# Performance work log

Measured on AMD Instinct MI355X. Metric: run time of the kernel, lower is better.

## Reference

```python
import jax, jax.numpy as jnp
import numpy as np

N, R, D = 2048, 4, 256
TEMPERATURE = 1.0
CLAMP_MIN = 1e-8


def setup_inputs() -> dict:
    key = jax.random.key(0)
    a = jax.random.normal(key, (N, R, D), dtype=jnp.float32)
    return {"a": a}


def reference(a):
    n, r, d = a.shape
    # Full pairwise Gram tensor over (input i, context j) x (input k, context l)
    sim = jnp.einsum('ijd,kld->ikjl', a, a) / TEMPERATURE          # [N,N,r,r]
    # detached row-max over l for stability (matches sim.detach().max(-1, keepdim=True))
    sim_max = jax.lax.stop_gradient(jnp.max(sim, axis=-1, keepdims=True))
    dp = jnp.exp(sim - sim_max)                                    # [N,N,r,r]

    # Positive pairs: i == k, j != l
    diag = jnp.einsum('iijl->ijl', dp)                             # [N,r,r]
    offdiag_jl = ~jnp.eye(r, dtype=bool)                           # [r,r]
    sim_pos = jnp.sum(diag * offdiag_jl, axis=(1, 2)) / (r * (r - 1))  # [N]

    # Negative pairs: i != k, all (j,l); square then clamp, then per-i mean
    sq = jnp.maximum(jnp.square(dp), CLAMP_MIN)                    # [N,N,r,r]
    diag_sq = jnp.sum(jnp.maximum(jnp.square(diag), CLAMP_MIN), axis=(1, 2))  # [N]
    sim_neg = (jnp.sum(sq, axis=(1, 2, 3)) - diag_sq) / ((n - 1) * r * r)     # [N]

    lora_loss = -2.0 * sim_pos + sim_neg                           # [N]
    return jnp.mean(lora_loss)                                     # 'mean' reduction -> scalar
```

## Files before the change

### kernel.cpp

```cpp
#include <hip/hip_runtime.h>


#define PD   8192
#define KB   256
#define BM   128
#define BK   32
#define NIT  (KB / BK)

typedef __bf16 bf16x8 __attribute__((ext_vector_type(8)));
typedef float f32x4 __attribute__((ext_vector_type(4)));

__device__ __forceinline__ void gload16(const void* g, void* l) {
    __builtin_amdgcn_global_load_lds(
        (const __attribute__((address_space(1))) unsigned int*)g,
        (__attribute__((address_space(3))) unsigned int*)l, 16, 0, 0);
}

__device__ __forceinline__ int swz(int row) { return ((row >> 1) & 3) << 4; }

__device__ __forceinline__ float quadmax(float x) {
    int v = __builtin_amdgcn_mov_dpp(__builtin_bit_cast(int, x), 0xB1, 0xF, 0xF, true);
    float m = fmaxf(x, __builtin_bit_cast(float, v));
    v = __builtin_amdgcn_mov_dpp(__builtin_bit_cast(int, m), 0x4E, 0xF, 0xF, true);
    return fmaxf(m, __builtin_bit_cast(float, v));
}

__global__ __launch_bounds__(256)
void cvt_bf16(const float* __restrict__ A, __bf16* __restrict__ W,
              float* __restrict__ out) {
    const int idx = blockIdx.x * 256 + threadIdx.x;
    if (idx == 0) *out = 0.f;
    const float4 v0 = reinterpret_cast<const float4*>(A)[idx * 2];
    const float4 v1 = reinterpret_cast<const float4*>(A)[idx * 2 + 1];
    bf16x8 h;
    h[0] = (__bf16)v0.x; h[1] = (__bf16)v0.y; h[2] = (__bf16)v0.z; h[3] = (__bf16)v0.w;
    h[4] = (__bf16)v1.x; h[5] = (__bf16)v1.y; h[6] = (__bf16)v1.z; h[7] = (__bf16)v1.w;
    *reinterpret_cast<bf16x8*>(W + (size_t)idx * 8) = h;
}

__global__ __launch_bounds__(256)
void evd_mfma(const __bf16* __restrict__ W, float* __restrict__ out)
{
    __shared__ __bf16 lds[2][2][BM * BK];
    __shared__ float wsum[4];

    const int x = blockIdx.x, y = blockIdx.y;
    int bi, bk;
    if (x < 64 - y) { bi = y;      bk = y + x; }
    else            { bi = 63 - y; bk = x - 1; }

    const int tid = threadIdx.x;
    const int lane = tid & 63, wid = tid >> 6;
    const int wr = wid >> 1, wc = wid & 1;
    const int row0 = bi * BM, col0 = bk * BM;

    const int r0 = tid >> 2;
    const int r1 = 64 + r0;
    const int x0 = (tid & 3) * 16;
    const int ga0 = r0 * (KB * 2) + (x0 ^ swz(r0));
    const int ga1 = r1 * (KB * 2) + (x0 ^ swz(r1));
    const char* gAb = (const char*)(W + (size_t)row0 * KB);
    const char* gBb = (const char*)(W + (size_t)col0 * KB);
    const int ldsOff0 = wid * 1024;
    const int ldsOff1 = 4096 + wid * 1024;

    const int fr = lane & 15, kq = lane >> 4;
    int aOff[4], bOff[4];
#pragma unroll
    for (int m = 0; m < 4; ++m) {
        const int ra = wr * 64 + m * 16 + fr;
        const int rb = wc * 64 + m * 16 + fr;
        aOff[m] = ra * 64 + ((kq * 16) ^ swz(ra));
        bOff[m] = rb * 64 + ((kq * 16) ^ swz(rb));
    }

    f32x4 acc[4][4];
#pragma unroll
    for (int m = 0; m < 4; ++m)
#pragma unroll
        for (int n = 0; n < 4; ++n)
#pragma unroll
            for (int q = 0; q < 4; ++q) acc[m][n][q] = 0.f;

    auto stage = [&](int t, int b) {
        const int kbyte = t * (BK * 2);
        char* dA = (char*)&lds[b][0][0];
        char* dB = (char*)&lds[b][1][0];
        gload16(gAb + ga0 + kbyte, dA + ldsOff0);
        gload16(gAb + ga1 + kbyte, dA + ldsOff1);
        gload16(gBb + ga0 + kbyte, dB + ldsOff0);
        gload16(gBb + ga1 + kbyte, dB + ldsOff1);
    };

    stage(0, 0);
    stage(1, 1);

#pragma unroll
    for (int t = 0; t < NIT; ++t) {
        if (t == NIT - 1) asm volatile("s_waitcnt vmcnt(0)" ::: "memory");
        else              asm volatile("s_waitcnt vmcnt(4)" ::: "memory");
        __builtin_amdgcn_s_barrier();

        const char* baseA = (const char*)&lds[t & 1][0][0];
        const char* baseB = (const char*)&lds[t & 1][1][0];
        bf16x8 af[4], bfr[4];
#pragma unroll
        for (int m = 0; m < 4; ++m) {
            af[m]  = *(const bf16x8*)(baseA + aOff[m]);
            bfr[m] = *(const bf16x8*)(baseB + bOff[m]);
        }
        if (t + 2 < NIT) {
            asm volatile("s_waitcnt lgkmcnt(0)" ::: "memory");
            __builtin_amdgcn_s_barrier();
            stage(t + 2, t & 1);
        }
#pragma unroll
        for (int m = 0; m < 4; ++m)
#pragma unroll
            for (int n = 0; n < 4; ++n)
                acc[m][n] = __builtin_amdgcn_mfma_f32_16x16x32_bf16(af[m], bfr[n], acc[m][n], 0, 0, 0);
    }

    const float C_NEG = 1.0f / (2048.0f * 2047.0f * 16.0f);
    const float C_POS = 2.0f / (2048.0f * 12.0f);
    const float SCL = 2.0f * 1.4426950408889634f;
    const bool diag = (bi == bk);
    const bool ik = ((lane >> 4) == ((lane & 15) >> 2));
    float nsum = 0.f, psum = 0.f;

#pragma unroll
    for (int m = 0; m < 4; ++m) {
#pragma unroll
        for (int n = 0; n < 4; ++n) {
            float yv[4];
#pragma unroll
            for (int q = 0; q < 4; ++q) yv[q] = SCL * acc[m][n][q];
            const bool dfrag = diag && (wr == wc) && (m == n);
#pragma unroll
            for (int r = 0; r < 4; ++r) {
                const float d2 = yv[r] - quadmax(yv[r]);
                if (dfrag) {
                    const float dp = __builtin_amdgcn_exp2f(0.5f * d2);
                    if (ik) {
                        if (r != (lane & 3)) psum += dp;
                    } else {
                        nsum += fmaxf(dp * dp, 1e-8f);
                    }
                } else {
                    nsum += fmaxf(__builtin_amdgcn_exp2f(d2), 1e-8f);
                }
            }
            if (!diag) {
                const float ymax = fmaxf(fmaxf(fmaxf(yv[0], yv[1]), yv[2]), yv[3]);
#pragma unroll
                for (int r = 0; r < 4; ++r)
                    nsum += fmaxf(__builtin_amdgcn_exp2f(yv[r] - ymax), 1e-8f);
            }
        }
    }

    float contrib = C_NEG * nsum - C_POS * psum;

#pragma unroll
    for (int off = 32; off; off >>= 1) contrib += __shfl_down(contrib, off);
    if ((tid & 63) == 0) wsum[tid >> 6] = contrib;
    __syncthreads();
    if (tid == 0) atomicAdd(out, wsum[0] + wsum[1] + wsum[2] + wsum[3]);
}

extern "C" void kernel_launch(void* const* d_in, const int* in_sizes, int n_in,
                              void* d_out, int out_size, void* d_ws, size_t ws_size,
                              hipStream_t stream) {
    const float* A = (const float*)d_in[0];
    float* out = (float*)d_out;
    __bf16* W = (__bf16*)d_ws;
    cvt_bf16<<<(PD * KB / 8) / 256, 256, 0, stream>>>(A, W, out);
    dim3 grid(65, 32);
    evd_mfma<<<grid, 256, 0, stream>>>(W, out);
}
```

Measured before the change: 98.96 us.

## Pair adjacent column tiles per block sharing one A tile across eight waves

Each block now has 512 threads and computes two neighbouring 128x128 upper-triangle tiles that share the same row tile. The A tile is loaded into LDS once and serves both halves, which cuts global-to-LDS traffic per tile. A new block-id remap spreads work across XCDs, and s_setprio raises wave priority around the MFMA loop. The cost is more LDS per block (three tile slices per buffer), and some blocks carry an invalid right tile whose work is computed and then discarded.

New measurement: 92.82 us. 6.2% less time.

```diff
diff --git a/kernel.cpp b/kernel.cpp
--- a/kernel.cpp
+++ b/kernel.cpp
@@ -38,31 +38,48 @@
     *reinterpret_cast<bf16x8*>(W + (size_t)idx * 8) = h;
 }
 
-__global__ __launch_bounds__(256)
+__global__ __launch_bounds__(512)
 void evd_mfma(const __bf16* __restrict__ W, float* __restrict__ out)
 {
-    __shared__ __bf16 lds[2][2][BM * BK];
-    __shared__ float wsum[4];
-
-    const int x = blockIdx.x, y = blockIdx.y;
-    int bi, bk;
-    if (x < 64 - y) { bi = y;      bk = y + x; }
-    else            { bi = 63 - y; bk = x - 1; }
+    __shared__ __bf16 lds[2][3][BM * BK];
+    __shared__ float wsum[8];
+
+    const int nid = (blockIdx.z * gridDim.y + blockIdx.y) * gridDim.x + blockIdx.x;
+    const int id  = (nid & 7) * 132 + (nid >> 3);
+    const int xx  = id % 33;
+    const int yzq = id / 33;
+    const int yy  = yzq & 15;
+    const int zz  = yzq >> 4;
+    int rp, px;
+    if (xx < 32 - yy) { rp = yy;      px = xx; }
+    else              { rp = 31 - yy; px = xx - (32 - yy); }
+    const int bi  = 2 * rp + zz;
+    const int bkL = bi + 2 * px;
+    int bkR = bkL + 1;
+    const bool validR = (bkR < 64);
+    if (!validR) bkR = bkL;
 
     const int tid = threadIdx.x;
-    const int lane = tid & 63, wid = tid >> 6;
-    const int wr = wid >> 1, wc = wid & 1;
-    const int row0 = bi * BM, col0 = bk * BM;
-
-    const int r0 = tid >> 2;
-    const int r1 = 64 + r0;
-    const int x0 = (tid & 3) * 16;
-    const int ga0 = r0 * (KB * 2) + (x0 ^ swz(r0));
-    const int ga1 = r1 * (KB * 2) + (x0 ^ swz(r1));
-    const char* gAb = (const char*)(W + (size_t)row0 * KB);
-    const char* gBb = (const char*)(W + (size_t)col0 * KB);
-    const int ldsOff0 = wid * 1024;
-    const int ldsOff1 = 4096 + wid * 1024;
+    const int lane = tid & 63, w = tid >> 6;
+    const int g = w >> 2;
+    const int sub = w & 3, wr = sub >> 1, wc = sub & 1;
+    const int row0 = bi * BM;
+    const int bk   = g ? bkR : bkL;
+    const int col0 = bk * BM;
+    const bool valid = g ? validR : true;
+
+    const int ar = tid >> 2;
+    const int ax = (tid & 3) * 16;
+    const int gaA = (row0 + ar) * (KB * 2) + (ax ^ swz(ar));
+    const int t2  = tid & 255;
+    const int br0 = t2 >> 2, br1 = 64 + br0;
+    const int bx  = (t2 & 3) * 16;
+    const int colB = (w < 4 ? bkL : bkR) * BM;
+    const int gaB0 = (colB + br0) * (KB * 2) + (bx ^ swz(br0));
+    const int gaB1 = (colB + br1) * (KB * 2) + (bx ^ swz(br1));
+    const char* gW = (const char*)W;
+    const int dA = w * 1024;
+    const int dB = 8192 + g * 8192 + (w & 3) * 1024;
 
     const int fr = lane & 15, kq = lane >> 4;
     int aOff[4], bOff[4];
@@ -71,7 +88,7 @@
         const int ra = wr * 64 + m * 16 + fr;
         const int rb = wc * 64 + m * 16 + fr;
         aOff[m] = ra * 64 + ((kq * 16) ^ swz(ra));
-        bOff[m] = rb * 64 + ((kq * 16) ^ swz(rb));
+        bOff[m] = 8192 + g * 8192 + rb * 64 + ((kq * 16) ^ swz(rb));
     }
 
     f32x4 acc[4][4];
@@ -83,13 +100,11 @@
             for (int q = 0; q < 4; ++q) acc[m][n][q] = 0.f;
 
     auto stage = [&](int t, int b) {
-        const int kbyte = t * (BK * 2);
-        char* dA = (char*)&lds[b][0][0];
-        char* dB = (char*)&lds[b][1][0];
-        gload16(gAb + ga0 + kbyte, dA + ldsOff0);
-        gload16(gAb + ga1 + kbyte, dA + ldsOff1);
-        gload16(gBb + ga0 + kbyte, dB + ldsOff0);
-        gload16(gBb + ga1 + kbyte, dB + ldsOff1);
+        const int kb2 = t * (BK * 2);
+        char* base = (char*)&lds[b][0][0];
+        gload16(gW + gaA  + kb2, base + dA);
+        gload16(gW + gaB0 + kb2, base + dB);
+        gload16(gW + gaB1 + kb2, base + dB + 4096);
     };
 
     stage(0, 0);
@@ -98,27 +113,28 @@
 #pragma unroll
     for (int t = 0; t < NIT; ++t) {
         if (t == NIT - 1) asm volatile("s_waitcnt vmcnt(0)" ::: "memory");
-        else              asm volatile("s_waitcnt vmcnt(4)" ::: "memory");
+        else              asm volatile("s_waitcnt vmcnt(3)" ::: "memory");
         __builtin_amdgcn_s_barrier();
 
-        const char* baseA = (const char*)&lds[t & 1][0][0];
-        const char* baseB = (const char*)&lds[t & 1][1][0];
+        const char* base = (const char*)&lds[t & 1][0][0];
         bf16x8 af[4], bfr[4];
 #pragma unroll
         for (int m = 0; m < 4; ++m) {
-            af[m]  = *(const bf16x8*)(baseA + aOff[m]);
-            bfr[m] = *(const bf16x8*)(baseB + bOff[m]);
+            af[m]  = *(const bf16x8*)(base + aOff[m]);
+            bfr[m] = *(const bf16x8*)(base + bOff[m]);
         }
         if (t + 2 < NIT) {
             asm volatile("s_waitcnt lgkmcnt(0)" ::: "memory");
             __builtin_amdgcn_s_barrier();
             stage(t + 2, t & 1);
         }
+        __builtin_amdgcn_s_setprio(1);
 #pragma unroll
         for (int m = 0; m < 4; ++m)
 #pragma unroll
             for (int n = 0; n < 4; ++n)
                 acc[m][n] = __builtin_amdgcn_mfma_f32_16x16x32_bf16(af[m], bfr[n], acc[m][n], 0, 0, 0);
+        __builtin_amdgcn_s_setprio(0);
     }
 
     const float C_NEG = 1.0f / (2048.0f * 2047.0f * 16.0f);
@@ -159,13 +175,18 @@
         }
     }
 
-    float contrib = C_NEG * nsum - C_POS * psum;
+    float contrib = valid ? (C_NEG * nsum - C_POS * psum) : 0.f;
 
 #pragma unroll
     for (int off = 32; off; off >>= 1) contrib += __shfl_down(contrib, off);
-    if ((tid & 63) == 0) wsum[tid >> 6] = contrib;
+    if (lane == 0) wsum[w] = contrib;
     __syncthreads();
-    if (tid == 0) atomicAdd(out, wsum[0] + wsum[1] + wsum[2] + wsum[3]);
+    if (tid == 0) {
+        float s = 0.f;
+#pragma unroll
+        for (int i = 0; i < 8; ++i) s += wsum[i];
+        atomicAdd(out, s);
+    }
 }
 
 extern "C" void kernel_launch(void* const* d_in, const int* in_sizes, int n_in,
@@ -175,6 +196,6 @@
     float* out = (float*)d_out;
     __bf16* W = (__bf16*)d_ws;
     cvt_bf16<<<(PD * KB / 8) / 256, 256, 0, stream>>>(A, W, out);
-    dim3 grid(65, 32);
-    evd_mfma<<<grid, 256, 0, stream>>>(W, out);
-}
+    dim3 grid(33, 16, 2);
+    evd_mfma<<<grid, 512, 0, stream>>>(W, out);
+}
```

## Stage K in two 128-wide halves with XOR swizzle and remapped block order

Applied to the files above, without the earlier changes.

Replaces the 8-step BK=32 double-buffered K loop with two large 128-wide K stages. Each stage fills a 64KB LDS buffer using an XOR-by-row swizzle, and the second half's loads are issued after the last fragment reads of the first half. Block IDs are remapped so that consecutive workgroups spread across groups of 8, which may improve L2/XCD locality. MFMA sections are wrapped in s_setprio. The trade-off is less overlap, since the first stage is fully exposed and the second overlaps only one MFMA group, and the larger LDS footprint may lower occupancy.

After: 97.16 us. Within noise of the previous version (-1.8%).

```diff
diff --git a/kernel.cpp b/kernel.cpp
--- a/kernel.cpp
+++ b/kernel.cpp
@@ -4,8 +4,7 @@
 #define PD   8192
 #define KB   256
 #define BM   128
-#define BK   32
-#define NIT  (KB / BK)
+#define KH   128
 
 typedef __bf16 bf16x8 __attribute__((ext_vector_type(8)));
 typedef float f32x4 __attribute__((ext_vector_type(4)));
@@ -15,8 +14,6 @@
         (const __attribute__((address_space(1))) unsigned int*)g,
         (__attribute__((address_space(3))) unsigned int*)l, 16, 0, 0);
 }
-
-__device__ __forceinline__ int swz(int row) { return ((row >> 1) & 3) << 4; }
 
 __device__ __forceinline__ float quadmax(float x) {
     int v = __builtin_amdgcn_mov_dpp(__builtin_bit_cast(int, x), 0xB1, 0xF, 0xF, true);
@@ -41,10 +38,12 @@
 __global__ __launch_bounds__(256)
 void evd_mfma(const __bf16* __restrict__ W, float* __restrict__ out)
 {
-    __shared__ __bf16 lds[2][2][BM * BK];
+    __shared__ __bf16 lds[2][BM * KH];
     __shared__ float wsum[4];
 
-    const int x = blockIdx.x, y = blockIdx.y;
+    const int nid = blockIdx.y * 65 + blockIdx.x;
+    const int id  = (nid & 7) * 260 + (nid >> 3);
+    const int x = id % 65, y = id / 65;
     int bi, bk;
     if (x < 64 - y) { bi = y;      bk = y + x; }
     else            { bi = 63 - y; bk = x - 1; }
@@ -54,24 +53,16 @@
     const int wr = wid >> 1, wc = wid & 1;
     const int row0 = bi * BM, col0 = bk * BM;
 
-    const int r0 = tid >> 2;
-    const int r1 = 64 + r0;
-    const int x0 = (tid & 3) * 16;
-    const int ga0 = r0 * (KB * 2) + (x0 ^ swz(r0));
-    const int ga1 = r1 * (KB * 2) + (x0 ^ swz(r1));
-    const char* gAb = (const char*)(W + (size_t)row0 * KB);
-    const char* gBb = (const char*)(W + (size_t)col0 * KB);
-    const int ldsOff0 = wid * 1024;
-    const int ldsOff1 = 4096 + wid * 1024;
+    const int srow = wid * 32 + (lane >> 4);
+    const int sunit = lane & 15;
+    const char* gW = (const char*)W;
 
     const int fr = lane & 15, kq = lane >> 4;
-    int aOff[4], bOff[4];
+    int aBase[4], bBase[4];
 #pragma unroll
     for (int m = 0; m < 4; ++m) {
-        const int ra = wr * 64 + m * 16 + fr;
-        const int rb = wc * 64 + m * 16 + fr;
-        aOff[m] = ra * 64 + ((kq * 16) ^ swz(ra));
-        bOff[m] = rb * 64 + ((kq * 16) ^ swz(rb));
+        aBase[m] = (wr * 64 + m * 16 + fr) * 256;
+        bBase[m] = 32768 + (wc * 64 + m * 16 + fr) * 256;
     }
 
     f32x4 acc[4][4];
@@ -82,43 +73,59 @@
 #pragma unroll
             for (int q = 0; q < 4; ++q) acc[m][n][q] = 0.f;
 
-    auto stage = [&](int t, int b) {
-        const int kbyte = t * (BK * 2);
-        char* dA = (char*)&lds[b][0][0];
-        char* dB = (char*)&lds[b][1][0];
-        gload16(gAb + ga0 + kbyte, dA + ldsOff0);
-        gload16(gAb + ga1 + kbyte, dA + ldsOff1);
-        gload16(gBb + ga0 + kbyte, dB + ldsOff0);
-        gload16(gBb + ga1 + kbyte, dB + ldsOff1);
+    auto stage = [&](int h) {
+        const int hb = h * (KH * 2);
+#pragma unroll
+        for (int i = 0; i < 8; ++i) {
+            const int r = srow + i * 4;
+            const int gu = ((sunit ^ (r & 15)) * 16);
+            gload16(gW + (size_t)(row0 + r) * (KB * 2) + hb + gu,
+                    (char*)lds + wid * 8192 + i * 1024);
+            gload16(gW + (size_t)(col0 + r) * (KB * 2) + hb + gu,
+                    (char*)lds + 32768 + wid * 8192 + i * 1024);
+        }
     };
 
-    stage(0, 0);
-    stage(1, 1);
-
-#pragma unroll
-    for (int t = 0; t < NIT; ++t) {
-        if (t == NIT - 1) asm volatile("s_waitcnt vmcnt(0)" ::: "memory");
-        else              asm volatile("s_waitcnt vmcnt(4)" ::: "memory");
-        __builtin_amdgcn_s_barrier();
-
-        const char* baseA = (const char*)&lds[t & 1][0][0];
-        const char* baseB = (const char*)&lds[t & 1][1][0];
-        bf16x8 af[4], bfr[4];
+    auto readFrags = [&](int ks, bf16x8* af, bf16x8* bfr) {
+        const int u = ((ks * 4 + kq) ^ fr) * 16;
 #pragma unroll
         for (int m = 0; m < 4; ++m) {
-            af[m]  = *(const bf16x8*)(baseA + aOff[m]);
-            bfr[m] = *(const bf16x8*)(baseB + bOff[m]);
+            af[m]  = *(const bf16x8*)((const char*)lds + aBase[m] + u);
+            bfr[m] = *(const bf16x8*)((const char*)lds + bBase[m] + u);
         }
-        if (t + 2 < NIT) {
-            asm volatile("s_waitcnt lgkmcnt(0)" ::: "memory");
-            __builtin_amdgcn_s_barrier();
-            stage(t + 2, t & 1);
-        }
+    };
+    auto mfma16 = [&](const bf16x8* af, const bf16x8* bfr) {
+        __builtin_amdgcn_s_setprio(1);
 #pragma unroll
         for (int m = 0; m < 4; ++m)
 #pragma unroll
             for (int n = 0; n < 4; ++n)
                 acc[m][n] = __builtin_amdgcn_mfma_f32_16x16x32_bf16(af[m], bfr[n], acc[m][n], 0, 0, 0);
+        __builtin_amdgcn_s_setprio(0);
+    };
+
+    stage(0);
+    __syncthreads();
+    {
+        bf16x8 af[4], bfr[4];
+#pragma unroll
+        for (int ks = 0; ks < 3; ++ks) {
+            readFrags(ks, af, bfr);
+            mfma16(af, bfr);
+        }
+        readFrags(3, af, bfr);
+        __syncthreads();
+        stage(1);
+        mfma16(af, bfr);
+    }
+    __syncthreads();
+    {
+        bf16x8 af[4], bfr[4];
+#pragma unroll
+        for (int ks = 0; ks < 4; ++ks) {
+            readFrags(ks, af, bfr);
+            mfma16(af, bfr);
+        }
     }
 
     const float C_NEG = 1.0f / (2048.0f * 2047.0f * 16.0f);
```

## Drop LDS staging; each wave computes its own 64x64 triangular tile from global loads

Applied to the files above, without the earlier changes.

Replaces the block-level 128x128 tile with LDS double-buffering by per-wave independent 64x64 upper-triangular tiles. Each wave loads MFMA fragments directly from global memory into registers with register double-buffering, which removes the LDS traffic and barriers. Blocks are remapped with an XCD-aware swizzle over a 1D grid of 2064 blocks, and s_setprio is raised around the MFMA bursts. In exchange, every wave reads its operands straight from global/L2 with no sharing between waves, so global read traffic rises.

After: 127.0 us. +28.3%, slower.

```diff
diff --git a/kernel.cpp b/kernel.cpp
--- a/kernel.cpp
+++ b/kernel.cpp
@@ -3,20 +3,10 @@
 
 #define PD   8192
 #define KB   256
-#define BM   128
-#define BK   32
-#define NIT  (KB / BK)
+#define NIT  8
 
 typedef __bf16 bf16x8 __attribute__((ext_vector_type(8)));
 typedef float f32x4 __attribute__((ext_vector_type(4)));
-
-__device__ __forceinline__ void gload16(const void* g, void* l) {
-    __builtin_amdgcn_global_load_lds(
-        (const __attribute__((address_space(1))) unsigned int*)g,
-        (__attribute__((address_space(3))) unsigned int*)l, 16, 0, 0);
-}
-
-__device__ __forceinline__ int swz(int row) { return ((row >> 1) & 3) << 4; }
 
 __device__ __forceinline__ float quadmax(float x) {
     int v = __builtin_amdgcn_mov_dpp(__builtin_bit_cast(int, x), 0xB1, 0xF, 0xF, true);
@@ -41,37 +31,27 @@
 __global__ __launch_bounds__(256)
 void evd_mfma(const __bf16* __restrict__ W, float* __restrict__ out)
 {
-    __shared__ __bf16 lds[2][2][BM * BK];
     __shared__ float wsum[4];
-
-    const int x = blockIdx.x, y = blockIdx.y;
-    int bi, bk;
-    if (x < 64 - y) { bi = y;      bk = y + x; }
-    else            { bi = 63 - y; bk = x - 1; }
 
     const int tid = threadIdx.x;
     const int lane = tid & 63, wid = tid >> 6;
-    const int wr = wid >> 1, wc = wid & 1;
-    const int row0 = bi * BM, col0 = bk * BM;
 
-    const int r0 = tid >> 2;
-    const int r1 = 64 + r0;
-    const int x0 = (tid & 3) * 16;
-    const int ga0 = r0 * (KB * 2) + (x0 ^ swz(r0));
-    const int ga1 = r1 * (KB * 2) + (x0 ^ swz(r1));
-    const char* gAb = (const char*)(W + (size_t)row0 * KB);
-    const char* gBb = (const char*)(W + (size_t)col0 * KB);
-    const int ldsOff0 = wid * 1024;
-    const int ldsOff1 = 4096 + wid * 1024;
+    const int nid = blockIdx.x;
+    const int id  = (nid & 7) * 258 + (nid >> 3);
+    const int gwid = id * 4 + wid;
+    const int p = gwid % 129, q = gwid / 129;
+    int bi, bk;
+    if (p < 128 - q) { bi = q;       bk = q + p; }
+    else             { bi = 127 - q; bk = (127 - q) + (p - (128 - q)); }
+    const int row0 = bi * 64, col0 = bk * 64;
 
     const int fr = lane & 15, kq = lane >> 4;
-    int aOff[4], bOff[4];
+    const char* aPtr[4];
+    const char* bPtr[4];
 #pragma unroll
     for (int m = 0; m < 4; ++m) {
-        const int ra = wr * 64 + m * 16 + fr;
-        const int rb = wc * 64 + m * 16 + fr;
-        aOff[m] = ra * 64 + ((kq * 16) ^ swz(ra));
-        bOff[m] = rb * 64 + ((kq * 16) ^ swz(rb));
+        aPtr[m] = (const char*)(W + (size_t)(row0 + m * 16 + fr) * KB + kq * 8);
+        bPtr[m] = (const char*)(W + (size_t)(col0 + m * 16 + fr) * KB + kq * 8);
     }
 
     f32x4 acc[4][4];
@@ -80,45 +60,31 @@
 #pragma unroll
         for (int n = 0; n < 4; ++n)
 #pragma unroll
-            for (int q = 0; q < 4; ++q) acc[m][n][q] = 0.f;
+            for (int q2 = 0; q2 < 4; ++q2) acc[m][n][q2] = 0.f;
 
-    auto stage = [&](int t, int b) {
-        const int kbyte = t * (BK * 2);
-        char* dA = (char*)&lds[b][0][0];
-        char* dB = (char*)&lds[b][1][0];
-        gload16(gAb + ga0 + kbyte, dA + ldsOff0);
-        gload16(gAb + ga1 + kbyte, dA + ldsOff1);
-        gload16(gBb + ga0 + kbyte, dB + ldsOff0);
-        gload16(gBb + ga1 + kbyte, dB + ldsOff1);
-    };
-
-    stage(0, 0);
-    stage(1, 1);
-
+    bf16x8 af[2][4], bf[2][4];
+#pragma unroll
+    for (int m = 0; m < 4; ++m) {
+        af[0][m] = *(const bf16x8*)(aPtr[m]);
+        bf[0][m] = *(const bf16x8*)(bPtr[m]);
+    }
 #pragma unroll
     for (int t = 0; t < NIT; ++t) {
-        if (t == NIT - 1) asm volatile("s_waitcnt vmcnt(0)" ::: "memory");
-        else              asm volatile("s_waitcnt vmcnt(4)" ::: "memory");
-        __builtin_amdgcn_s_barrier();
-
-        const char* baseA = (const char*)&lds[t & 1][0][0];
-        const char* baseB = (const char*)&lds[t & 1][1][0];
-        bf16x8 af[4], bfr[4];
+        if (t + 1 < NIT) {
 #pragma unroll
-        for (int m = 0; m < 4; ++m) {
-            af[m]  = *(const bf16x8*)(baseA + aOff[m]);
-            bfr[m] = *(const bf16x8*)(baseB + bOff[m]);
+            for (int m = 0; m < 4; ++m) {
+                af[(t + 1) & 1][m] = *(const bf16x8*)(aPtr[m] + (t + 1) * 64);
+                bf[(t + 1) & 1][m] = *(const bf16x8*)(bPtr[m] + (t + 1) * 64);
+            }
         }
-        if (t + 2 < NIT) {
-            asm volatile("s_waitcnt lgkmcnt(0)" ::: "memory");
-            __builtin_amdgcn_s_barrier();
-            stage(t + 2, t & 1);
-        }
+        __builtin_amdgcn_s_setprio(1);
 #pragma unroll
         for (int m = 0; m < 4; ++m)
 #pragma unroll
             for (int n = 0; n < 4; ++n)
-                acc[m][n] = __builtin_amdgcn_mfma_f32_16x16x32_bf16(af[m], bfr[n], acc[m][n], 0, 0, 0);
+                acc[m][n] = __builtin_amdgcn_mfma_f32_16x16x32_bf16(
+                    af[t & 1][m], bf[t & 1][n], acc[m][n], 0, 0, 0);
+        __builtin_amdgcn_s_setprio(0);
     }
 
     const float C_NEG = 1.0f / (2048.0f * 2047.0f * 16.0f);
@@ -134,8 +100,8 @@
         for (int n = 0; n < 4; ++n) {
             float yv[4];
 #pragma unroll
-            for (int q = 0; q < 4; ++q) yv[q] = SCL * acc[m][n][q];
-            const bool dfrag = diag && (wr == wc) && (m == n);
+            for (int q2 = 0; q2 < 4; ++q2) yv[q2] = SCL * acc[m][n][q2];
+            const bool dfrag = diag && (m == n);
 #pragma unroll
             for (int r = 0; r < 4; ++r) {
                 const float d2 = yv[r] - quadmax(yv[r]);
@@ -163,7 +129,7 @@
 
 #pragma unroll
     for (int off = 32; off; off >>= 1) contrib += __shfl_down(contrib, off);
-    if ((tid & 63) == 0) wsum[tid >> 6] = contrib;
+    if (lane == 0) wsum[wid] = contrib;
     __syncthreads();
     if (tid == 0) atomicAdd(out, wsum[0] + wsum[1] + wsum[2] + wsum[3]);
 }
@@ -175,6 +141,5 @@
     float* out = (float*)d_out;
     __bf16* W = (__bf16*)d_ws;
     cvt_bf16<<<(PD * KB / 8) / 256, 256, 0, stream>>>(A, W, out);
-    dim3 grid(65, 32);
-    evd_mfma<<<grid, 256, 0, stream>>>(W, out);
+    evd_mfma<<<2064, 256, 0, stream>>>(W, out);
 }
```
